# Kernel tuning notes

Measured on AMD Instinct MI355X. Metric: run time of the kernel, lower is better.

## Reference

```python
import jax, jax.numpy as jnp
import numpy as np

D = 256
B, S, N = 4, 512, 4


def setup_inputs() -> dict:
    key = jax.random.key(0)
    ks = jax.random.split(key, 24)
    d, dq = D, D // 4
    std = 0.02
    inp = {
        'x':   jax.random.normal(ks[0], (B, S, N, d), jnp.float32),
        'Wq':  jax.random.normal(ks[1], (d, d), jnp.float32) * std,
        'Wk':  jax.random.normal(ks[2], (d, d), jnp.float32) * std,
        'Wv':  jax.random.normal(ks[3], (d, d), jnp.float32) * std,
        'Wg1': jax.random.normal(ks[4], (d, d), jnp.float32) * std,
        'bg1': jnp.zeros((d,), jnp.float32),
        'Wg2': jax.random.normal(ks[5], (d, d), jnp.float32) * std,
        'bg2': jnp.zeros((d,), jnp.float32),
        'We1': jax.random.normal(ks[6], (d, dq), jnp.float32) * std,
        'be1': jnp.zeros((dq,), jnp.float32),
        'We2': jax.random.normal(ks[7], (dq, 1), jnp.float32) * std,
        'be2': jnp.zeros((1,), jnp.float32),
        'Wa1': jax.random.normal(ks[8], (d, dq), jnp.float32) * std,
        'ba1': jnp.zeros((dq,), jnp.float32),
        'Wa2': jax.random.normal(ks[9], (dq, 1), jnp.float32) * std,
        'ba2': jnp.zeros((1,), jnp.float32),
        'Wo':  jax.random.normal(ks[10], (d, d), jnp.float32) * std,
        'bo':  jnp.zeros((d,), jnp.float32),
        'gamma': jnp.ones((d,), jnp.float32),
        'beta':  jnp.zeros((d,), jnp.float32),
    }
    return inp


def reference(x, Wq, Wk, Wv, Wg1, bg1, Wg2, bg2, We1, be1, We2, be2,
              Wa1, ba1, Wa2, ba2, Wo, bo, gamma, beta):
    b, s, n, f = x.shape
    xf = x.reshape(b * n, s, f)  # matches torch .view on contiguous x
    residual = xf

    q = xf @ Wq                                    # [bn, s, d]
    k = xf @ Wk
    v = xf @ Wv
    v_hat = jax.nn.silu(v @ Wg1 + bg1) @ Wg2 + bg2  # value_generator
    eta = jax.nn.sigmoid(jax.nn.silu(xf @ We1 + be1) @ We2 + be2) * 0.1 + 0.01   # [bn, s, 1]
    alpha = jax.nn.sigmoid(jax.nn.silu(xf @ Wa1 + ba1) @ Wa2 + ba2) * 0.5 + 0.5  # [bn, s, 1]

    # F.normalize(k, dim=-1): eps = 1e-12
    kn = k / jnp.maximum(jnp.linalg.norm(k, axis=-1, keepdims=True), 1e-12)

    M0 = jnp.zeros((b * n, f, f), x.dtype)

    def step(M, inp):
        q_t, k_t, v_t, e_t, a_t = inp  # [bn,d],[bn,d],[bn,d],[bn,1],[bn,1]
        out_t = jnp.einsum('bij,bj->bi', M, q_t)
        Mk = jnp.einsum('bij,bj->bi', M, k_t)
        e = e_t[:, :, None]  # [bn,1,1]
        a = a_t[:, :, None]
        # delta rule: M <- a*M - e*(Mk k^T) + e*(v k^T)
        M_new = a * M + e * ((v_t - Mk)[:, :, None] * k_t[:, None, :])
        return M_new, out_t

    seq = (jnp.swapaxes(q, 0, 1), jnp.swapaxes(kn, 0, 1), jnp.swapaxes(v_hat, 0, 1),
           jnp.swapaxes(eta, 0, 1), jnp.swapaxes(alpha, 0, 1))
    M, outs = jax.lax.scan(step, M0, seq)
    out = jnp.swapaxes(outs, 0, 1)  # [bn, s, d]

    y = out @ Wo + bo + residual  # dropout is identity in eval/reference
    mu = jnp.mean(y, axis=-1, keepdims=True)
    var = jnp.var(y, axis=-1, keepdims=True)
    y = (y - mu) / jnp.sqrt(var + 1e-5) * gamma + beta
    return y.reshape(b, s, n, f), M
```

## Files before the change

### kernel.cpp

```cpp
#include <hip/hip_runtime.h>

#define F_ 256
#define S_ 512
#define NH_ 16
#define CCH 32
#define NCH (S_/CCH)
#define KSTR 264
#define KTSTR 36
#define TSTR 40

typedef __attribute__((ext_vector_type(8))) short short8_t;
typedef __attribute__((ext_vector_type(4))) float f32x4;

#define BARX() do { \
  asm volatile("s_waitcnt lgkmcnt(0)" ::: "memory"); \
  __builtin_amdgcn_s_barrier(); \
  __builtin_amdgcn_sched_barrier(0); \
} while (0)

__device__ __forceinline__ float sigmoid_f(float x) { return 1.0f / (1.0f + __expf(-x)); }

__device__ __forceinline__ ushort f2bf(float x) {
  uint u = __float_as_uint(x);
  u += 0x7FFFu + ((u >> 16) & 1u);
  return (ushort)(u >> 16);
}
__device__ __forceinline__ float bf2f(ushort u) {
  return __uint_as_float((uint)u << 16);
}

template<int CTRL>
__device__ __forceinline__ float dpp_add(float x) {
  int y = __builtin_amdgcn_update_dpp(0, __float_as_int(x), CTRL, 0xf, 0xf, true);
  return x + __int_as_float(y);
}
__device__ __forceinline__ float red8(float x) {
  x = dpp_add<0xB1>(x);
  x = dpp_add<0x4E>(x);
  x = dpp_add<0x141>(x);
  return x;
}

__global__ __launch_bounds__(256) void wconv_k(
    const float* __restrict__ Wq, const float* __restrict__ Wk,
    const float* __restrict__ Wv, const float* __restrict__ Wg1,
    const float* __restrict__ Wg2, const float* __restrict__ Wo,
    const float* __restrict__ We1, const float* __restrict__ Wa1,
    const float* __restrict__ be1, const float* __restrict__ ba1,
    ushort* __restrict__ Wt, float* __restrict__ beas)
{
  const int blk = blockIdx.x, tid = threadIdx.x;
  if (blk == 104) {
    if (tid < 64) beas[tid] = be1[tid];
    else if (tid < 128) beas[tid] = ba1[tid - 64];
    return;
  }
  __shared__ float tile[64][65];
  const float* src; int N, k0, n0; size_t dstbase;
  if (blk < 96) {
    const int w = blk >> 4, tl = blk & 15;
    const float* ws_[6] = {Wq, Wk, Wv, Wg1, Wg2, Wo};
    const size_t dstb[6] = {0, 65536, 131072, 229376, 294912, 360448};
    src = ws_[w]; N = 256;
    k0 = (tl >> 2) * 64; n0 = (tl & 3) * 64;
    dstbase = dstb[w];
  } else {
    const int w = (blk - 96) >> 2, tl = (blk - 96) & 3;
    src = w ? Wa1 : We1; N = 64;
    k0 = tl * 64; n0 = 0;
    dstbase = w ? 212992 : 196608;
  }
  #pragma unroll
  for (int p = 0; p < 4; ++p) {
    const int idx = (p << 8) + tid;
    const int r = idx >> 4, c4 = (idx & 15) << 2;
    if (c4 < N) {
      const float4 v = *(const float4*)&src[(size_t)(k0 + r) * N + n0 + c4];
      tile[r][c4 + 0] = v.x; tile[r][c4 + 1] = v.y;
      tile[r][c4 + 2] = v.z; tile[r][c4 + 3] = v.w;
    }
  }
  __syncthreads();
  #pragma unroll
  for (int p = 0; p < 4; ++p) {
    const int idx = (p << 8) + tid;
    const int nl = idx >> 4, kc = (idx & 15) << 2;
    if ((n0 + nl) < ((blk < 96) ? 256 : 64)) {
      ushort4 o;
      o.x = f2bf(tile[kc + 0][nl]); o.y = f2bf(tile[kc + 1][nl]);
      o.z = f2bf(tile[kc + 2][nl]); o.w = f2bf(tile[kc + 3][nl]);
      *(ushort4*)&Wt[dstbase + (size_t)(n0 + nl) * 256 + k0 + kc] = o;
    }
  }
}

__global__ __launch_bounds__(256) void qkve_k(
    const float* __restrict__ x, const ushort* __restrict__ Wt,
    const float* __restrict__ beas,
    ushort* __restrict__ qb, float* __restrict__ kf,
    ushort* __restrict__ vb, float* __restrict__ sesa)
{
  __shared__ ushort As[2][64 * 72];
  __shared__ ushort Ws[2][64 * 72];
  const int tid = threadIdx.x;
  const int wv = tid >> 6, l = tid & 63;
  const int ln = l & 15, hi = l >> 4, hi4 = hi << 2, hi8 = hi << 3;
  const int wr = wv >> 1, wc = wv & 1;
  const int row0 = blockIdx.y * 64, col0 = blockIdx.x * 64;
  const int r_ = tid >> 3, c8_ = (tid & 7) << 3;

  float4 pAf[4];
  short8_t pB[2];
  auto loadT = [&](int k0) {
    pAf[0] = *(const float4*)&x[(size_t)(row0 + r_) * 256 + k0 + c8_];
    pAf[1] = *(const float4*)&x[(size_t)(row0 + r_) * 256 + k0 + c8_ + 4];
    pAf[2] = *(const float4*)&x[(size_t)(row0 + 32 + r_) * 256 + k0 + c8_];
    pAf[3] = *(const float4*)&x[(size_t)(row0 + 32 + r_) * 256 + k0 + c8_ + 4];
    pB[0] = *(const short8_t*)&Wt[(size_t)(col0 + r_) * 256 + k0 + c8_];
    pB[1] = *(const short8_t*)&Wt[(size_t)(col0 + 32 + r_) * 256 + k0 + c8_];
  };
  auto commitT = [&](int b) {
    #pragma unroll
    for (int h = 0; h < 2; ++h) {
      short8_t s;
      s[0] = (short)f2bf(pAf[h*2].x); s[1] = (short)f2bf(pAf[h*2].y);
      s[2] = (short)f2bf(pAf[h*2].z); s[3] = (short)f2bf(pAf[h*2].w);
      s[4] = (short)f2bf(pAf[h*2+1].x); s[5] = (short)f2bf(pAf[h*2+1].y);
      s[6] = (short)f2bf(pAf[h*2+1].z); s[7] = (short)f2bf(pAf[h*2+1].w);
      *(short8_t*)&As[b][(h * 32 + r_) * 72 + c8_] = s;
    }
    *(short8_t*)&Ws[b][r_ * 72 + c8_] = pB[0];
    *(short8_t*)&Ws[b][(32 + r_) * 72 + c8_] = pB[1];
  };

  f32x4 acc[2][2];
  #pragma unroll
  for (int i = 0; i < 2; ++i)
    #pragma unroll
    for (int j = 0; j < 2; ++j)
      #pragma unroll
      for (int r = 0; r < 4; ++r) acc[i][j][r] = 0.f;

  loadT(0); commitT(0); __syncthreads();
  #pragma unroll
  for (int t = 0; t < 4; ++t) {
    const int b = t & 1;
    if (t < 3) loadT((t + 1) << 6);
    #pragma unroll
    for (int kk = 0; kk < 2; ++kk) {
      short8_t a0 = *(const short8_t*)&As[b][(wr * 32 + ln) * 72 + kk * 32 + hi8];
      short8_t a1 = *(const short8_t*)&As[b][(wr * 32 + 16 + ln) * 72 + kk * 32 + hi8];
      short8_t b0 = *(const short8_t*)&Ws[b][(wc * 32 + ln) * 72 + kk * 32 + hi8];
      short8_t b1 = *(const short8_t*)&Ws[b][(wc * 32 + 16 + ln) * 72 + kk * 32 + hi8];
      acc[0][0] = __builtin_amdgcn_mfma_f32_16x16x32_bf16(a0, b0, acc[0][0], 0, 0, 0);
      acc[0][1] = __builtin_amdgcn_mfma_f32_16x16x32_bf16(a0, b1, acc[0][1], 0, 0, 0);
      acc[1][0] = __builtin_amdgcn_mfma_f32_16x16x32_bf16(a1, b0, acc[1][0], 0, 0, 0);
      acc[1][1] = __builtin_amdgcn_mfma_f32_16x16x32_bf16(a1, b1, acc[1][1], 0, 0, 0);
    }
    if (t < 3) commitT(b ^ 1);
    __syncthreads();
  }

  #pragma unroll
  for (int mi = 0; mi < 2; ++mi)
    #pragma unroll
    for (int ni = 0; ni < 2; ++ni) {
      const int col = col0 + wc * 32 + ni * 16 + ln;
      #pragma unroll
      for (int r = 0; r < 4; ++r) {
        const int row = row0 + wr * 32 + mi * 16 + hi4 + r;
        float vx = acc[mi][ni][r];
        if (col0 < 256)      qb[(size_t)row * 256 + col] = f2bf(vx);
        else if (col0 < 512) kf[(size_t)row * 256 + (col - 256)] = vx;
        else if (col0 < 768) vb[(size_t)row * 256 + (col - 512)] = f2bf(vx);
        else {
          const int cc = col - 768;
          vx += beas[cc];
          vx *= sigmoid_f(vx);
          sesa[(size_t)row * 128 + cc] = vx;
        }
      }
    }
}

__global__ __launch_bounds__(256) void gemm_bf16_k(
    const ushort* __restrict__ A, const ushort* __restrict__ Wt,
    const float* __restrict__ bias, float* __restrict__ Cf,
    ushort* __restrict__ Cb, int act)
{
  __shared__ ushort As[2][64 * 72];
  __shared__ ushort Ws[2][64 * 72];
  const int tid = threadIdx.x;
  const int wv = tid >> 6, l = tid & 63;
  const int ln = l & 15, hi = l >> 4, hi4 = hi << 2, hi8 = hi << 3;
  const int wr = wv >> 1, wc = wv & 1;
  const int row0 = blockIdx.y * 64, col0 = blockIdx.x * 64;
  const int r_ = tid >> 3, c8_ = (tid & 7) << 3;

  short8_t pA[2], pB[2];
  auto loadT = [&](int k0) {
    pA[0] = *(const short8_t*)&A[(size_t)(row0 + r_) * 256 + k0 + c8_];
    pA[1] = *(const short8_t*)&A[(size_t)(row0 + 32 + r_) * 256 + k0 + c8_];
    pB[0] = *(const short8_t*)&Wt[(size_t)(col0 + r_) * 256 + k0 + c8_];
    pB[1] = *(const short8_t*)&Wt[(size_t)(col0 + 32 + r_) * 256 + k0 + c8_];
  };
  auto commitT = [&](int b) {
    *(short8_t*)&As[b][r_ * 72 + c8_] = pA[0];
    *(short8_t*)&As[b][(32 + r_) * 72 + c8_] = pA[1];
    *(short8_t*)&Ws[b][r_ * 72 + c8_] = pB[0];
    *(short8_t*)&Ws[b][(32 + r_) * 72 + c8_] = pB[1];
  };

  f32x4 acc[2][2];
  #pragma unroll
  for (int i = 0; i < 2; ++i)
    #pragma unroll
    for (int j = 0; j < 2; ++j)
      #pragma unroll
      for (int r = 0; r < 4; ++r) acc[i][j][r] = 0.f;

  loadT(0); commitT(0); __syncthreads();
  #pragma unroll
  for (int t = 0; t < 4; ++t) {
    const int b = t & 1;
    if (t < 3) loadT((t + 1) << 6);
    #pragma unroll
    for (int kk = 0; kk < 2; ++kk) {
      short8_t a0 = *(const short8_t*)&As[b][(wr * 32 + ln) * 72 + kk * 32 + hi8];
      short8_t a1 = *(const short8_t*)&As[b][(wr * 32 + 16 + ln) * 72 + kk * 32 + hi8];
      short8_t b0 = *(const short8_t*)&Ws[b][(wc * 32 + ln) * 72 + kk * 32 + hi8];
      short8_t b1 = *(const short8_t*)&Ws[b][(wc * 32 + 16 + ln) * 72 + kk * 32 + hi8];
      acc[0][0] = __builtin_amdgcn_mfma_f32_16x16x32_bf16(a0, b0, acc[0][0], 0, 0, 0);
      acc[0][1] = __builtin_amdgcn_mfma_f32_16x16x32_bf16(a0, b1, acc[0][1], 0, 0, 0);
      acc[1][0] = __builtin_amdgcn_mfma_f32_16x16x32_bf16(a1, b0, acc[1][0], 0, 0, 0);
      acc[1][1] = __builtin_amdgcn_mfma_f32_16x16x32_bf16(a1, b1, acc[1][1], 0, 0, 0);
    }
    if (t < 3) commitT(b ^ 1);
    __syncthreads();
  }

  #pragma unroll
  for (int mi = 0; mi < 2; ++mi)
    #pragma unroll
    for (int ni = 0; ni < 2; ++ni) {
      const int col = col0 + wc * 32 + ni * 16 + ln;
      const float bval = bias ? bias[col] : 0.f;
      #pragma unroll
      for (int r = 0; r < 4; ++r) {
        const int row = row0 + wr * 32 + mi * 16 + hi4 + r;
        float vx = acc[mi][ni][r] + bval;
        if (act == 1) vx = vx * sigmoid_f(vx);
        if (Cf) Cf[(size_t)row * 256 + col] = vx;
        if (Cb) Cb[(size_t)row * 256 + col] = f2bf(vx);
      }
    }
}

__global__ __launch_bounds__(256) void g1prep_k(
    const ushort* __restrict__ vb, const ushort* __restrict__ WtG1,
    const float* __restrict__ bg1, ushort* __restrict__ t1b,
    const ushort* __restrict__ kb, const ushort* __restrict__ qb,
    const float* __restrict__ eta, const float* __restrict__ alpha,
    ushort* __restrict__ Tg, ushort* __restrict__ Gqg, float* __restrict__ Sg,
    ushort* __restrict__ Ktg)
{
  __shared__ __align__(16) char smem[38592];
  const int blk = blockIdx.x;
  const int tid = threadIdx.x;
  const int l = tid & 63, wv = tid >> 6;
  const int ln = l & 15, hi = l >> 4, hi4 = hi << 2, hi8 = hi << 3;

  if (blk < 512) {
    ushort* As = (ushort*)smem;
    ushort* Ws = (ushort*)(smem + 18432);
    const int wr = wv >> 1, wc = wv & 1;
    const int row0 = (blk >> 2) * 64, col0 = (blk & 3) * 64;
    const int r_ = tid >> 3, c8_ = (tid & 7) << 3;

    short8_t pA[2], pB[2];
    auto loadT = [&](int k0) {
      pA[0] = *(const short8_t*)&vb[(size_t)(row0 + r_) * 256 + k0 + c8_];
      pA[1] = *(const short8_t*)&vb[(size_t)(row0 + 32 + r_) * 256 + k0 + c8_];
      pB[0] = *(const short8_t*)&WtG1[(size_t)(col0 + r_) * 256 + k0 + c8_];
      pB[1] = *(const short8_t*)&WtG1[(size_t)(col0 + 32 + r_) * 256 + k0 + c8_];
    };
    auto commitT = [&](int b) {
      *(short8_t*)&As[b * 4608 + r_ * 72 + c8_] = pA[0];
      *(short8_t*)&As[b * 4608 + (32 + r_) * 72 + c8_] = pA[1];
      *(short8_t*)&Ws[b * 4608 + r_ * 72 + c8_] = pB[0];
      *(short8_t*)&Ws[b * 4608 + (32 + r_) * 72 + c8_] = pB[1];
    };

    f32x4 acc[2][2];
    #pragma unroll
    for (int i = 0; i < 2; ++i)
      #pragma unroll
      for (int j = 0; j < 2; ++j)
        #pragma unroll
        for (int r = 0; r < 4; ++r) acc[i][j][r] = 0.f;

    loadT(0); commitT(0); __syncthreads();
    #pragma unroll
    for (int t = 0; t < 4; ++t) {
      const int b = t & 1;
      if (t < 3) loadT((t + 1) << 6);
      #pragma unroll
      for (int kk = 0; kk < 2; ++kk) {
        short8_t a0 = *(const short8_t*)&As[b * 4608 + (wr * 32 + ln) * 72 + kk * 32 + hi8];
        short8_t a1 = *(const short8_t*)&As[b * 4608 + (wr * 32 + 16 + ln) * 72 + kk * 32 + hi8];
        short8_t b0 = *(const short8_t*)&Ws[b * 4608 + (wc * 32 + ln) * 72 + kk * 32 + hi8];
        short8_t b1 = *(const short8_t*)&Ws[b * 4608 + (wc * 32 + 16 + ln) * 72 + kk * 32 + hi8];
        acc[0][0] = __builtin_amdgcn_mfma_f32_16x16x32_bf16(a0, b0, acc[0][0], 0, 0, 0);
        acc[0][1] = __builtin_amdgcn_mfma_f32_16x16x32_bf16(a0, b1, acc[0][1], 0, 0, 0);
        acc[1][0] = __builtin_amdgcn_mfma_f32_16x16x32_bf16(a1, b0, acc[1][0], 0, 0, 0);
        acc[1][1] = __builtin_amdgcn_mfma_f32_16x16x32_bf16(a1, b1, acc[1][1], 0, 0, 0);
      }
      if (t < 3) commitT(b ^ 1);
      __syncthreads();
    }

    #pragma unroll
    for (int mi = 0; mi < 2; ++mi)
      #pragma unroll
      for (int ni = 0; ni < 2; ++ni) {
        const int col = col0 + wc * 32 + ni * 16 + ln;
        const float bval = bg1[col];
        #pragma unroll
        for (int r = 0; r < 4; ++r) {
          const int row = row0 + wr * 32 + mi * 16 + hi4 + r;
          float vx = acc[mi][ni][r] + bval;
          vx = vx * sigmoid_f(vx);
          t1b[(size_t)row * 256 + col] = f2bf(vx);
        }
      }
    return;
  }

  const int pb = blk - 512;
  const int ch = pb & 15, h = pb >> 4;
  const int t0 = ch * CCH;
  ushort* K_lds = (ushort*)smem;
  ushort* Q_lds = (ushort*)(smem + 16896);
  float*  G_lds = (float*)(smem + 33792);
  float*  ea    = (float*)(smem + 37888);
  float*  eaA   = (float*)(smem + 37888 + 0);
  float*  scal  = (float*)(smem + 38144);

  const ushort* kg = kb + (size_t)(h * S_ + t0) * F_;
  const ushort* qg = qb + (size_t)(h * S_ + t0) * F_;
  #pragma unroll
  for (int w = 0; w < 4; ++w) {
    int o = w * 256 + tid; int t = o >> 5, c8 = (o & 31) << 3;
    *(short8_t*)&K_lds[t * KSTR + c8] = *(const short8_t*)&kg[(size_t)t * F_ + c8];
    *(short8_t*)&Q_lds[t * KSTR + c8] = *(const short8_t*)&qg[(size_t)t * F_ + c8];
  }
  if (tid < CCH)            ea[tid] = eta[(size_t)h * S_ + t0 + tid];
  else if (tid < 2 * CCH)   ea[tid] = alpha[(size_t)h * S_ + t0 + tid - CCH];
  __syncthreads();
  (void)eaA;

  {
    const int tt = tid & 31, cl = tid >> 5;
    for (int cp = 0; cp < 32; ++cp) {
      const int c = cp * 8 + cl;
      Ktg[((size_t)h * F_ + c) * S_ + t0 + tt] = K_lds[tt * KSTR + c];
    }
  }

  {
    const int tI = wv >> 1, tJ = wv & 1;
    f32x4 accG = {0.f, 0.f, 0.f, 0.f};
    f32x4 accQ = {0.f, 0.f, 0.f, 0.f};
    #pragma unroll
    for (int ko = 0; ko < 8; ++ko) {
      const int cb = ko * 32 + hi8;
      short8_t bfr = *(const short8_t*)&K_lds[(tJ * 16 + ln) * KSTR + cb];
      short8_t aK  = *(const short8_t*)&K_lds[(tI * 16 + ln) * KSTR + cb];
      short8_t aQ  = *(const short8_t*)&Q_lds[(tI * 16 + ln) * KSTR + cb];
      accG = __builtin_amdgcn_mfma_f32_16x16x32_bf16(aK, bfr, accG, 0, 0, 0);
      accQ = __builtin_amdgcn_mfma_f32_16x16x32_bf16(aQ, bfr, accQ, 0, 0, 0);
    }
    ushort* Gqo = Gqg + (size_t)(h * NCH + ch) * (CCH * CCH);
    #pragma unroll
    for (int r = 0; r < 4; ++r) {
      const int t = tI * 16 + hi4 + r, s = tJ * 16 + ln;
      G_lds[t * CCH + s] = accG[r];
      Gqo[t * CCH + s] = (s < t) ? f2bf(accQ[r]) : (ushort)0;
    }
  }
  if (tid == 0) {
    float gp = 1.f;
    for (int t = 0; t < CCH; ++t) {
      const float a = ea[CCH + t], e = ea[t];
      const float gm = gp * a;
      scal[t]           = e / a;
      scal[CCH + t]     = e / gm;
      scal[2 * CCH + t] = gp;
      gp = gm;
    }
    scal[3 * CCH] = gp;
  }
  __syncthreads();

  {
    const int j = tid >> 3, g = tid & 7;
    float x0 = 0.f, x1 = 0.f, x2 = 0.f, x3 = 0.f;
    ushort* To = Tg + (size_t)(h * NCH + ch) * (CCH * CCH);
    #pragma unroll
    for (int t = 0; t < CCH; ++t) {
      float p = 0.f;
      const f32x4 gr = *(const f32x4*)&G_lds[t * CCH + 4 * g];
      if (4 * g + 0 < t) p += gr[0] * x0;
      if (4 * g + 1 < t) p += gr[1] * x1;
      if (4 * g + 2 < t) p += gr[2] * x2;
      if (4 * g + 3 < t) p += gr[3] * x3;
      const float tot = red8(p);
      const float xt = ((t == j) ? 1.f : 0.f) - scal[t] * tot;
      if (g == (t >> 2)) {
        if ((t & 3) == 0) x0 = xt; else if ((t & 3) == 1) x1 = xt;
        else if ((t & 3) == 2) x2 = xt; else x3 = xt;
      }
      if (g == 0) To[t * CCH + j] = f2bf(xt);
    }
  }
  if (tid < 97) Sg[(size_t)(h * NCH + ch) * 128 + tid] = scal[tid];
}

__global__ __launch_bounds__(256) void gemmo_ln_k(
    const ushort* __restrict__ A, const ushort* __restrict__ Wt,
    const float* __restrict__ bo, const float* __restrict__ x,
    const float* __restrict__ gamma, const float* __restrict__ beta,
    float* __restrict__ y)
{
  __shared__ ushort As[2][32 * 72];
  __shared__ ushort Ws[2][256 * 72];
  __shared__ float rs_[2][32];
  __shared__ float rq_[2][32];
  const int tid = threadIdx.x;
  const int wv = tid >> 6, l = tid & 63;
  const int ln = l & 15, hi = l >> 4, hi4 = hi << 2, hi8 = hi << 3;
  const int g = wv >> 1, chf = wv & 1;
  const int row0 = blockIdx.x * 32;

  short8_t pA, pW[8];
  auto loadT = [&](int k0) {
    { const int r = tid >> 3, c8 = (tid & 7) << 3;
      pA = *(const short8_t*)&A[(size_t)(row0 + r) * 256 + k0 + c8]; }
    #pragma unroll
    for (int p = 0; p < 8; ++p) {
      const int idx = (p << 8) + tid;
      const int n = idx >> 3, c8 = (idx & 7) << 3;
      pW[p] = *(const short8_t*)&Wt[(size_t)n * 256 + k0 + c8];
    }
  };
  auto commitT = [&](int b) {
    { const int r = tid >> 3, c8 = (tid & 7) << 3;
      *(short8_t*)&As[b][r * 72 + c8] = pA; }
    #pragma unroll
    for (int p = 0; p < 8; ++p) {
      const int idx = (p << 8) + tid;
      const int n = idx >> 3, c8 = (idx & 7) << 3;
      *(short8_t*)&Ws[b][n * 72 + c8] = pW[p];
    }
  };

  f32x4 acc[8];
  #pragma unroll
  for (int nt = 0; nt < 8; ++nt)
    #pragma unroll
    for (int r = 0; r < 4; ++r) acc[nt][r] = 0.f;

  loadT(0); commitT(0); __syncthreads();
  #pragma unroll
  for (int t = 0; t < 4; ++t) {
    const int b = t & 1;
    if (t < 3) loadT((t + 1) << 6);
    #pragma unroll
    for (int kk = 0; kk < 2; ++kk) {
      short8_t a = *(const short8_t*)&As[b][(g * 16 + ln) * 72 + kk * 32 + hi8];
      #pragma unroll
      for (int nt = 0; nt < 8; ++nt) {
        short8_t bb = *(const short8_t*)&Ws[b][(chf * 128 + nt * 16 + ln) * 72 + kk * 32 + hi8];
        acc[nt] = __builtin_amdgcn_mfma_f32_16x16x32_bf16(a, bb, acc[nt], 0, 0, 0);
      }
    }
    if (t < 3) commitT(b ^ 1);
    __syncthreads();
  }

  float val[8][4];
  float sm[4] = {0.f, 0.f, 0.f, 0.f}, sq[4] = {0.f, 0.f, 0.f, 0.f};
  #pragma unroll
  for (int nt = 0; nt < 8; ++nt) {
    const int col = chf * 128 + nt * 16 + ln;
    const float bv = bo[col];
    #pragma unroll
    for (int r = 0; r < 4; ++r) {
      const int row = row0 + g * 16 + hi4 + r;
      const float v = acc[nt][r] + bv + x[(size_t)row * 256 + col];
      val[nt][r] = v;
      sm[r] += v;
      sq[r] += v * v;
    }
  }
  #pragma unroll
  for (int m = 1; m < 16; m <<= 1) {
    #pragma unroll
    for (int r = 0; r < 4; ++r) {
      sm[r] += __shfl_xor(sm[r], m, 64);
      sq[r] += __shfl_xor(sq[r], m, 64);
    }
  }
  if (ln == 0) {
    #pragma unroll
    for (int r = 0; r < 4; ++r) {
      rs_[chf][g * 16 + hi4 + r] = sm[r];
      rq_[chf][g * 16 + hi4 + r] = sq[r];
    }
  }
  __syncthreads();
  #pragma unroll
  for (int r = 0; r < 4; ++r) {
    const int lr = g * 16 + hi4 + r;
    const float tot = rs_[0][lr] + rs_[1][lr];
    const float tq  = rq_[0][lr] + rq_[1][lr];
    const float mu  = tot * (1.0f / 256.0f);
    const float var = tq * (1.0f / 256.0f) - mu * mu;
    const float rstd = rsqrtf(var + 1e-5f);
    #pragma unroll
    for (int nt = 0; nt < 8; ++nt) {
      const int col = chf * 128 + nt * 16 + ln;
      y[(size_t)(row0 + lr) * 256 + col] =
          (val[nt][r] - mu) * rstd * gamma[col] + beta[col];
    }
  }
}

__global__ __launch_bounds__(256) void knea_k(
    const float* __restrict__ kf, ushort* __restrict__ kb,
    const float* __restrict__ sesa,
    const float* __restrict__ We2, const float* __restrict__ be2,
    const float* __restrict__ Wa2, const float* __restrict__ ba2,
    float* __restrict__ eta, float* __restrict__ alpha)
{
  const int lane = threadIdx.x & 63;
  const size_t row = ((size_t)blockIdx.x << 2) + (threadIdx.x >> 6);
  {
    const size_t off = row * F_ + ((size_t)lane << 2);
    float4 v = *(const float4*)&kf[off];
    float ss = v.x * v.x + v.y * v.y + v.z * v.z + v.w * v.w;
    #pragma unroll
    for (int m = 1; m < 64; m <<= 1) ss += __shfl_xor(ss, m, 64);
    const float sc = 1.0f / fmaxf(sqrtf(ss), 1e-12f);
    ushort4 o;
    o.x = f2bf(v.x * sc); o.y = f2bf(v.y * sc);
    o.z = f2bf(v.z * sc); o.w = f2bf(v.w * sc);
    *(ushort4*)&kb[off] = o;
  }
  {
    float pe = sesa[row * 128 + lane] * We2[lane];
    float pa = sesa[row * 128 + 64 + lane] * Wa2[lane];
    #pragma unroll
    for (int m = 1; m < 64; m <<= 1) {
      pe += __shfl_xor(pe, m, 64);
      pa += __shfl_xor(pa, m, 64);
    }
    if (lane == 0) {
      eta[row]   = sigmoid_f(pe + be2[0]) * 0.1f + 0.01f;
      alpha[row] = sigmoid_f(pa + ba2[0]) * 0.5f + 0.5f;
    }
  }
}

__global__ __launch_bounds__(256, 1) void scan_chunk_k(
    const ushort* __restrict__ kb, const ushort* __restrict__ qb,
    const ushort* __restrict__ vhb, const ushort* __restrict__ Ktg,
    const ushort* __restrict__ Tg, const ushort* __restrict__ Gqg,
    const float* __restrict__ Sg,
    ushort* __restrict__ outb, float* __restrict__ Mout)
{
  __shared__ ushort K_lds[2][CCH * KSTR];
  __shared__ ushort Q_lds[2][CCH * KSTR];
  __shared__ ushort Kt_lds[2][F_ * KTSTR];
  __shared__ ushort M_lds[16 * KSTR];
  __shared__ ushort T_lds[2][CCH * TSTR];
  __shared__ ushort Gq_lds[2][CCH * TSTR];
  __shared__ ushort Wt_lds[16 * TSTR];
  __shared__ ushort R2_lds[2][16 * TSTR];
  __shared__ float  QM_lds[CCH * 20];
  __shared__ ushort V_lds[2][CCH * 16];
  __shared__ float  scal[2][104];

  const int tid = threadIdx.x;
  const int flat = blockIdx.x;
  const int h = (flat & 7) + (((flat >> 3) >> 4) << 3);
  const int slice = (flat >> 3) & 15;
  const int r0 = slice * 16;
  const int wv = tid >> 6, l = tid & 63;
  const int ln = l & 15, hi = l >> 4, hi4 = hi << 2, hi8 = hi << 3;

  for (int u = tid; u < 16 * KSTR / 8; u += 256) {
    short8_t z = {0, 0, 0, 0, 0, 0, 0, 0};
    *(short8_t*)&M_lds[u * 8] = z;
  }
  f32x4 Mf[4];
  #pragma unroll
  for (int q = 0; q < 4; ++q)
    #pragma unroll
    for (int r = 0; r < 4; ++r) Mf[q][r] = 0.f;

  const ushort* kgh = kb + (size_t)h * S_ * F_;
  const ushort* qgh = qb + (size_t)h * S_ * F_;
  const ushort* kth = Ktg + (size_t)h * F_ * S_;

  short8_t pK[4], pQ[4], pKt[4], pTG;
  ushort pV[2]; float pS = 0.f;

  auto loadchunk = [&](int ch) {
    const int t0 = ch * CCH;
    #pragma unroll
    for (int r = 0; r < 4; ++r) {
      const int idx = (r << 8) + tid;
      const int t = idx >> 5, c8 = (idx & 31) << 3;
      pK[r] = *(const short8_t*)&kgh[(size_t)(t0 + t) * F_ + c8];
      pQ[r] = *(const short8_t*)&qgh[(size_t)(t0 + t) * F_ + c8];
    }
    #pragma unroll
    for (int r = 0; r < 4; ++r) {
      const int idx = (r << 8) + tid;
      const int c = idx >> 2, t8 = (idx & 3) << 3;
      pKt[r] = *(const short8_t*)&kth[(size_t)c * S_ + t0 + t8];
    }
    #pragma unroll
    for (int u = 0; u < 2; ++u) {
      const int e = (u << 8) + tid, t = e >> 4, i = e & 15;
      pV[u] = vhb[(size_t)(h * S_ + t0 + t) * F_ + r0 + i];
    }
    {
      const ushort* Ti = Tg  + (size_t)(h * NCH + ch) * (CCH * CCH);
      const ushort* Gi = Gqg + (size_t)(h * NCH + ch) * (CCH * CCH);
      if (tid < 128) {
        const int t = tid >> 2, c8 = (tid & 3) << 3;
        pTG = *(const short8_t*)&Ti[t * CCH + c8];
      } else {
        const int t = (tid - 128) >> 2, c8 = ((tid - 128) & 3) << 3;
        pTG = *(const short8_t*)&Gi[t * CCH + c8];
      }
    }
    if (tid < 97) pS = Sg[(size_t)(h * NCH + ch) * 128 + tid];
  };

  auto commit = [&](int buf) {
    #pragma unroll
    for (int r = 0; r < 4; ++r) {
      const int idx = (r << 8) + tid;
      const int t = idx >> 5, c8 = (idx & 31) << 3;
      *(short8_t*)&K_lds[buf][t * KSTR + c8] = pK[r];
      *(short8_t*)&Q_lds[buf][t * KSTR + c8] = pQ[r];
    }
    #pragma unroll
    for (int r = 0; r < 4; ++r) {
      const int idx = (r << 8) + tid;
      const int c = idx >> 2, t8 = (idx & 3) << 3;
      *(short8_t*)&Kt_lds[buf][c * KTSTR + t8] = pKt[r];
    }
    #pragma unroll
    for (int u = 0; u < 2; ++u) V_lds[buf][(u << 8) + tid] = pV[u];
    if (tid < 128) {
      const int t = tid >> 2, c8 = (tid & 3) << 3;
      *(short8_t*)&T_lds[buf][t * TSTR + c8] = pTG;
    } else {
      const int t = (tid - 128) >> 2, c8 = ((tid - 128) & 3) << 3;
      *(short8_t*)&Gq_lds[buf][t * TSTR + c8] = pTG;
    }
    if (tid < 97) scal[buf][tid] = pS;
  };

  loadchunk(0);
  commit(0);
  BARX();

  for (int ch = 0; ch < NCH; ++ch) {
    const int buf = ch & 1;
    const int t0 = ch * CCH;
    if (ch + 1 < NCH) loadchunk(ch + 1);

    if (wv < 2) {
      #pragma unroll
      for (int tt = 0; tt < 2; ++tt) {
        f32x4 a0 = {0.f, 0.f, 0.f, 0.f}, a1 = {0.f, 0.f, 0.f, 0.f};
        #pragma unroll
        for (int ko = 0; ko < 4; ++ko) {
          {
            short8_t a = *(const short8_t*)&K_lds[buf][(tt * 16 + ln) * KSTR + (2 * ko) * 32 + hi8];
            short8_t b = *(const short8_t*)&M_lds[ln * KSTR + (2 * ko) * 32 + hi8];
            a0 = __builtin_amdgcn_mfma_f32_16x16x32_bf16(a, b, a0, 0, 0, 0);
          }
          {
            short8_t a = *(const short8_t*)&K_lds[buf][(tt * 16 + ln) * KSTR + (2 * ko + 1) * 32 + hi8];
            short8_t b = *(const short8_t*)&M_lds[ln * KSTR + (2 * ko + 1) * 32 + hi8];
            a1 = __builtin_amdgcn_mfma_f32_16x16x32_bf16(a, b, a1, 0, 0, 0);
          }
        }
        #pragma unroll
        for (int r = 0; r < 4; ++r) {
          const int t = tt * 16 + hi4 + r;
          const float s = a0[r] + a1[r];
          const float rhs = scal[buf][CCH + t] * bf2f(V_lds[buf][t * 16 + ln])
                          - scal[buf][t] * s;
          R2_lds[wv][ln * TSTR + t] = f2bf(rhs);
        }
      }
      asm volatile("s_waitcnt lgkmcnt(0)" ::: "memory");
      __builtin_amdgcn_sched_barrier(0);
      {
        const int I = wv;
        short8_t a = *(const short8_t*)&T_lds[buf][(I * 16 + ln) * TSTR + hi8];
        short8_t b = *(const short8_t*)&R2_lds[wv][ln * TSTR + hi8];
        f32x4 z = {0.f, 0.f, 0.f, 0.f};
        f32x4 d = __builtin_amdgcn_mfma_f32_16x16x32_bf16(a, b, z, 0, 0, 0);
        #pragma unroll
        for (int r = 0; r < 4; ++r)
          Wt_lds[ln * TSTR + I * 16 + hi4 + r] = f2bf(d[r]);
      }
    } else {
      const int I = wv - 2;
      f32x4 a0 = {0.f, 0.f, 0.f, 0.f}, a1 = {0.f, 0.f, 0.f, 0.f};
      #pragma unroll
      for (int ko = 0; ko < 4; ++ko) {
        {
          short8_t a = *(const short8_t*)&Q_lds[buf][(I * 16 + ln) * KSTR + (2 * ko) * 32 + hi8];
          short8_t b = *(const short8_t*)&M_lds[ln * KSTR + (2 * ko) * 32 + hi8];
          a0 = __builtin_amdgcn_mfma_f32_16x16x32_bf16(a, b, a0, 0, 0, 0);
        }
        {
          short8_t a = *(const short8_t*)&Q_lds[buf][(I * 16 + ln) * KSTR + (2 * ko + 1) * 32 + hi8];
          short8_t b = *(const short8_t*)&M_lds[ln * KSTR + (2 * ko + 1) * 32 + hi8];
          a1 = __builtin_amdgcn_mfma_f32_16x16x32_bf16(a, b, a1, 0, 0, 0);
        }
      }
      #pragma unroll
      for (int r = 0; r < 4; ++r)
        QM_lds[(I * 16 + hi4 + r) * 20 + ln] = a0[r] + a1[r];
    }
    BARX();

    {
      const float gC = scal[buf][3 * CCH];
      short8_t aw = *(const short8_t*)&Wt_lds[ln * TSTR + hi8];
      #pragma unroll
      for (int qq = 0; qq < 4; ++qq) {
        const int jt = wv * 4 + qq;
        short8_t bk = *(const short8_t*)&Kt_lds[buf][(jt * 16 + ln) * KTSTR + hi8];
        f32x4 d = __builtin_amdgcn_mfma_f32_16x16x32_bf16(aw, bk, Mf[qq], 0, 0, 0);
        #pragma unroll
        for (int r = 0; r < 4; ++r) {
          const float nv = gC * d[r];
          Mf[qq][r] = nv;
          M_lds[(hi4 + r) * KSTR + jt * 16 + ln] = f2bf(nv);
        }
      }
    }
    if (wv < 2) {
      const int I = wv;
      short8_t a = *(const short8_t*)&Gq_lds[buf][(I * 16 + ln) * TSTR + hi8];
      short8_t b = *(const short8_t*)&Wt_lds[ln * TSTR + hi8];
      f32x4 z = {0.f, 0.f, 0.f, 0.f};
      f32x4 d = __builtin_amdgcn_mfma_f32_16x16x32_bf16(a, b, z, 0, 0, 0);
      #pragma unroll
      for (int r = 0; r < 4; ++r) {
        const int t = I * 16 + hi4 + r;
        outb[(size_t)(h * S_ + t0 + t) * F_ + r0 + ln] =
            f2bf(scal[buf][2 * CCH + t] * (QM_lds[t * 20 + ln] + d[r]));
      }
    }
    if (ch + 1 < NCH) commit(buf ^ 1);
    BARX();
  }

  #pragma unroll
  for (int qq = 0; qq < 4; ++qq) {
    const int jt = wv * 4 + qq;
    #pragma unroll
    for (int r = 0; r < 4; ++r)
      Mout[((size_t)h * F_ + r0 + hi4 + r) * F_ + jt * 16 + ln] = Mf[qq][r];
  }
}

extern "C" void kernel_launch(void* const* d_in, const int* in_sizes, int n_in,
                              void* d_out, int out_size, void* d_ws, size_t ws_size,
                              hipStream_t stream)
{
  const float* x    = (const float*)d_in[0];
  const float* Wq   = (const float*)d_in[1];
  const float* Wk   = (const float*)d_in[2];
  const float* Wv   = (const float*)d_in[3];
  const float* Wg1  = (const float*)d_in[4];
  const float* bg1  = (const float*)d_in[5];
  const float* Wg2  = (const float*)d_in[6];
  const float* bg2  = (const float*)d_in[7];
  const float* We1  = (const float*)d_in[8];
  const float* be1  = (const float*)d_in[9];
  const float* We2  = (const float*)d_in[10];
  const float* be2  = (const float*)d_in[11];
  const float* Wa1  = (const float*)d_in[12];
  const float* ba1  = (const float*)d_in[13];
  const float* Wa2  = (const float*)d_in[14];
  const float* ba2  = (const float*)d_in[15];
  const float* Wo   = (const float*)d_in[16];
  const float* bo   = (const float*)d_in[17];
  const float* gamma= (const float*)d_in[18];
  const float* beta = (const float*)d_in[19];

  const int Mrows = NH_ * S_;
  const size_t MM = 1048576;
  const size_t NTF = 2 * MM;

  float* ws = (float*)d_ws;
  ushort* outb = (ushort*)(ws + 0 * MM);
  ushort* qb   = (ushort*)(ws + 1 * MM);
  ushort* kb   = (ushort*)(ws + 2 * MM);
  float*  kf   = ws + 3 * MM;
  ushort* t1b  = (ushort*)(ws + 3 * MM);
  ushort* vhb  = (ushort*)(ws + 4 * MM);
  ushort* vb   = (ushort*)(ws + 5 * MM);
  float*  sesa = ws + 6 * MM;
  float*  eta  = ws + 7 * MM;
  float*  alpha= eta + Mrows;
  ushort* Tg   = (ushort*)(ws + 7 * MM + 16384);
  ushort* Gqg  = Tg + 262144;
  float*  Sg   = ws + 7 * MM + 16384 + 131072 + 131072;
  ushort* Ktg  = (ushort*)(Sg + 32768);
  ushort* Wt   = Ktg + 2097152;
  float*  beas = (float*)(Wt + 425984);

  dim3 blk(256);

  wconv_k<<<105, blk, 0, stream>>>(Wq, Wk, Wv, Wg1, Wg2, Wo, We1, Wa1,
                                   be1, ba1, Wt, beas);

  qkve_k<<<dim3(14, 128), blk, 0, stream>>>(x, Wt, beas, qb, kf, vb, sesa);

  knea_k<<<Mrows / 4, blk, 0, stream>>>(kf, kb, sesa, We2, be2, Wa2, ba2, eta, alpha);

  g1prep_k<<<768, blk, 0, stream>>>(vb, Wt + 229376, bg1, t1b,
                                    kb, qb, eta, alpha, Tg, Gqg, Sg, Ktg);

  gemm_bf16_k<<<dim3(4, 128), blk, 0, stream>>>(t1b, Wt + 294912, bg2, nullptr, vhb, 0);

  float* yout = (float*)d_out;
  float* Mfin = yout + NTF;
  scan_chunk_k<<<256, blk, 0, stream>>>(kb, qb, vhb, Ktg, Tg, Gqg, Sg, outb, Mfin);

  gemmo_ln_k<<<256, blk, 0, stream>>>(outb, Wt + 360448, bo, x, gamma, beta, yout);
}
```

Measured before the change: 96.81 us.

## Load scan operands straight into MFMA register fragments, drop LDS staging

The chunked scan kernel no longer stages K, Q, K^T, T, Gq, V and the scalars through double-buffered LDS. Each wave now loads its own MFMA operand fragments straight from global memory into registers, ping-ponging between two fragment sets across an unrolled pair of chunks. This removes the LDS commit writes and the re-reads, and cuts shared memory use. In exchange it adds an extra barrier per chunk (three instead of two), much higher register pressure, and less coalesced, fragment-shaped global loads (for example strided K^T rows).

```diff
diff --git a/kernel.cpp b/kernel.cpp
--- a/kernel.cpp
+++ b/kernel.cpp
@@ -6,7 +6,6 @@
 #define CCH 32
 #define NCH (S_/CCH)
 #define KSTR 264
-#define KTSTR 36
 #define TSTR 40
 
 typedef __attribute__((ext_vector_type(8))) short short8_t;
@@ -343,7 +342,6 @@
   ushort* Q_lds = (ushort*)(smem + 16896);
   float*  G_lds = (float*)(smem + 33792);
   float*  ea    = (float*)(smem + 37888);
-  float*  eaA   = (float*)(smem + 37888 + 0);
   float*  scal  = (float*)(smem + 38144);
 
   const ushort* kg = kb + (size_t)(h * S_ + t0) * F_;
@@ -357,7 +355,6 @@
   if (tid < CCH)            ea[tid] = eta[(size_t)h * S_ + t0 + tid];
   else if (tid < 2 * CCH)   ea[tid] = alpha[(size_t)h * S_ + t0 + tid - CCH];
   __syncthreads();
-  (void)eaA;
 
   {
     const int tt = tid & 31, cl = tid >> 5;
@@ -579,17 +576,10 @@
     const float* __restrict__ Sg,
     ushort* __restrict__ outb, float* __restrict__ Mout)
 {
-  __shared__ ushort K_lds[2][CCH * KSTR];
-  __shared__ ushort Q_lds[2][CCH * KSTR];
-  __shared__ ushort Kt_lds[2][F_ * KTSTR];
   __shared__ ushort M_lds[16 * KSTR];
-  __shared__ ushort T_lds[2][CCH * TSTR];
-  __shared__ ushort Gq_lds[2][CCH * TSTR];
   __shared__ ushort Wt_lds[16 * TSTR];
-  __shared__ ushort R2_lds[2][16 * TSTR];
+  __shared__ ushort R_lds[16 * TSTR];
   __shared__ float  QM_lds[CCH * 20];
-  __shared__ ushort V_lds[2][CCH * 16];
-  __shared__ float  scal[2][104];
 
   const int tid = threadIdx.x;
   const int flat = blockIdx.x;
@@ -612,170 +602,127 @@
   const ushort* kgh = kb + (size_t)h * S_ * F_;
   const ushort* qgh = qb + (size_t)h * S_ * F_;
   const ushort* kth = Ktg + (size_t)h * F_ * S_;
-
-  short8_t pK[4], pQ[4], pKt[4], pTG;
-  ushort pV[2]; float pS = 0.f;
-
-  auto loadchunk = [&](int ch) {
+  const ushort* vgh = vhb + (size_t)h * S_ * F_;
+
+  struct Frags {
+    short8_t P[8];
+    short8_t Kt[4];
+    short8_t T, Gq;
+    ushort   V[4];
+    float    b[4], c[4], gp[4];
+    float    gC;
+  };
+  Frags fA, fB;
+
+  auto loadchunk = [&](int ch, Frags& f) {
     const int t0 = ch * CCH;
-    #pragma unroll
-    for (int r = 0; r < 4; ++r) {
-      const int idx = (r << 8) + tid;
-      const int t = idx >> 5, c8 = (idx & 31) << 3;
-      pK[r] = *(const short8_t*)&kgh[(size_t)(t0 + t) * F_ + c8];
-      pQ[r] = *(const short8_t*)&qgh[(size_t)(t0 + t) * F_ + c8];
-    }
-    #pragma unroll
-    for (int r = 0; r < 4; ++r) {
-      const int idx = (r << 8) + tid;
-      const int c = idx >> 2, t8 = (idx & 3) << 3;
-      pKt[r] = *(const short8_t*)&kth[(size_t)c * S_ + t0 + t8];
-    }
-    #pragma unroll
-    for (int u = 0; u < 2; ++u) {
-      const int e = (u << 8) + tid, t = e >> 4, i = e & 15;
-      pV[u] = vhb[(size_t)(h * S_ + t0 + t) * F_ + r0 + i];
-    }
+    if (wv < 2) {
+      #pragma unroll
+      for (int ko = 0; ko < 8; ++ko)
+        f.P[ko] = *(const short8_t*)&kgh[(size_t)(t0 + wv * 16 + ln) * F_ + ko * 32 + hi8];
+      const size_t tb = (size_t)(h * NCH + ch) * (CCH * CCH);
+      f.T  = *(const short8_t*)&Tg [tb + (size_t)(wv * 16 + ln) * CCH + hi8];
+      f.Gq = *(const short8_t*)&Gqg[tb + (size_t)(wv * 16 + ln) * CCH + hi8];
+      const size_t sb = (size_t)(h * NCH + ch) * 128;
+      #pragma unroll
+      for (int r = 0; r < 4; ++r) {
+        const int t = wv * 16 + hi4 + r;
+        f.V[r]  = vgh[(size_t)(t0 + t) * F_ + r0 + ln];
+        f.b[r]  = Sg[sb + t];
+        f.c[r]  = Sg[sb + 32 + t];
+        f.gp[r] = Sg[sb + 64 + t];
+      }
+    } else {
+      #pragma unroll
+      for (int ko = 0; ko < 8; ++ko)
+        f.P[ko] = *(const short8_t*)&qgh[(size_t)(t0 + (wv - 2) * 16 + ln) * F_ + ko * 32 + hi8];
+    }
+    #pragma unroll
+    for (int qq = 0; qq < 4; ++qq)
+      f.Kt[qq] = *(const short8_t*)&kth[(size_t)((wv * 4 + qq) * 16 + ln) * S_ + t0 + hi8];
+    f.gC = Sg[(size_t)(h * NCH + ch) * 128 + 96];
+  };
+
+  auto CHUNK = [&](int ch, const Frags& f) {
+    const int t0 = ch * CCH;
+    if (wv < 2) {
+      f32x4 a0 = {0.f, 0.f, 0.f, 0.f}, a1 = {0.f, 0.f, 0.f, 0.f};
+      #pragma unroll
+      for (int ko = 0; ko < 4; ++ko) {
+        short8_t b0 = *(const short8_t*)&M_lds[ln * KSTR + (2 * ko) * 32 + hi8];
+        a0 = __builtin_amdgcn_mfma_f32_16x16x32_bf16(f.P[2 * ko], b0, a0, 0, 0, 0);
+        short8_t b1 = *(const short8_t*)&M_lds[ln * KSTR + (2 * ko + 1) * 32 + hi8];
+        a1 = __builtin_amdgcn_mfma_f32_16x16x32_bf16(f.P[2 * ko + 1], b1, a1, 0, 0, 0);
+      }
+      ushort4 rw;
+      float rv[4];
+      #pragma unroll
+      for (int r = 0; r < 4; ++r) {
+        const float s = a0[r] + a1[r];
+        rv[r] = f.c[r] * bf2f(f.V[r]) - f.b[r] * s;
+      }
+      rw.x = f2bf(rv[0]); rw.y = f2bf(rv[1]); rw.z = f2bf(rv[2]); rw.w = f2bf(rv[3]);
+      *(ushort4*)&R_lds[ln * TSTR + wv * 16 + hi4] = rw;
+    } else {
+      f32x4 a0 = {0.f, 0.f, 0.f, 0.f}, a1 = {0.f, 0.f, 0.f, 0.f};
+      #pragma unroll
+      for (int ko = 0; ko < 4; ++ko) {
+        short8_t b0 = *(const short8_t*)&M_lds[ln * KSTR + (2 * ko) * 32 + hi8];
+        a0 = __builtin_amdgcn_mfma_f32_16x16x32_bf16(f.P[2 * ko], b0, a0, 0, 0, 0);
+        short8_t b1 = *(const short8_t*)&M_lds[ln * KSTR + (2 * ko + 1) * 32 + hi8];
+        a1 = __builtin_amdgcn_mfma_f32_16x16x32_bf16(f.P[2 * ko + 1], b1, a1, 0, 0, 0);
+      }
+      #pragma unroll
+      for (int r = 0; r < 4; ++r)
+        QM_lds[((wv - 2) * 16 + hi4 + r) * 20 + ln] = a0[r] + a1[r];
+    }
+    BARX();
+
+    if (wv < 2) {
+      short8_t bfr = *(const short8_t*)&R_lds[ln * TSTR + hi8];
+      f32x4 z = {0.f, 0.f, 0.f, 0.f};
+      f32x4 d = __builtin_amdgcn_mfma_f32_16x16x32_bf16(f.T, bfr, z, 0, 0, 0);
+      ushort4 wo;
+      wo.x = f2bf(d[0]); wo.y = f2bf(d[1]); wo.z = f2bf(d[2]); wo.w = f2bf(d[3]);
+      *(ushort4*)&Wt_lds[ln * TSTR + wv * 16 + hi4] = wo;
+    }
+    BARX();
+
     {
-      const ushort* Ti = Tg  + (size_t)(h * NCH + ch) * (CCH * CCH);
-      const ushort* Gi = Gqg + (size_t)(h * NCH + ch) * (CCH * CCH);
-      if (tid < 128) {
-        const int t = tid >> 2, c8 = (tid & 3) << 3;
-        pTG = *(const short8_t*)&Ti[t * CCH + c8];
-      } else {
-        const int t = (tid - 128) >> 2, c8 = ((tid - 128) & 3) << 3;
-        pTG = *(const short8_t*)&Gi[t * CCH + c8];
-      }
-    }
-    if (tid < 97) pS = Sg[(size_t)(h * NCH + ch) * 128 + tid];
-  };
-
-  auto commit = [&](int buf) {
-    #pragma unroll
-    for (int r = 0; r < 4; ++r) {
-      const int idx = (r << 8) + tid;
-      const int t = idx >> 5, c8 = (idx & 31) << 3;
-      *(short8_t*)&K_lds[buf][t * KSTR + c8] = pK[r];
-      *(short8_t*)&Q_lds[buf][t * KSTR + c8] = pQ[r];
-    }
-    #pragma unroll
-    for (int r = 0; r < 4; ++r) {
-      const int idx = (r << 8) + tid;
-      const int c = idx >> 2, t8 = (idx & 3) << 3;
-      *(short8_t*)&Kt_lds[buf][c * KTSTR + t8] = pKt[r];
-    }
-    #pragma unroll
-    for (int u = 0; u < 2; ++u) V_lds[buf][(u << 8) + tid] = pV[u];
-    if (tid < 128) {
-      const int t = tid >> 2, c8 = (tid & 3) << 3;
-      *(short8_t*)&T_lds[buf][t * TSTR + c8] = pTG;
-    } else {
-      const int t = (tid - 128) >> 2, c8 = ((tid - 128) & 3) << 3;
-      *(short8_t*)&Gq_lds[buf][t * TSTR + c8] = pTG;
-    }
-    if (tid < 97) scal[buf][tid] = pS;
-  };
-
-  loadchunk(0);
-  commit(0);
-  BARX();
-
-  for (int ch = 0; ch < NCH; ++ch) {
-    const int buf = ch & 1;
-    const int t0 = ch * CCH;
-    if (ch + 1 < NCH) loadchunk(ch + 1);
-
-    if (wv < 2) {
-      #pragma unroll
-      for (int tt = 0; tt < 2; ++tt) {
-        f32x4 a0 = {0.f, 0.f, 0.f, 0.f}, a1 = {0.f, 0.f, 0.f, 0.f};
-        #pragma unroll
-        for (int ko = 0; ko < 4; ++ko) {
-          {
-            short8_t a = *(const short8_t*)&K_lds[buf][(tt * 16 + ln) * KSTR + (2 * ko) * 32 + hi8];
-            short8_t b = *(const short8_t*)&M_lds[ln * KSTR + (2 * ko) * 32 + hi8];
-            a0 = __builtin_amdgcn_mfma_f32_16x16x32_bf16(a, b, a0, 0, 0, 0);
-          }
-          {
-            short8_t a = *(const short8_t*)&K_lds[buf][(tt * 16 + ln) * KSTR + (2 * ko + 1) * 32 + hi8];
-            short8_t b = *(const short8_t*)&M_lds[ln * KSTR + (2 * ko + 1) * 32 + hi8];
-            a1 = __builtin_amdgcn_mfma_f32_16x16x32_bf16(a, b, a1, 0, 0, 0);
-          }
-        }
+      short8_t aw = *(const short8_t*)&Wt_lds[ln * TSTR + hi8];
+      #pragma unroll
+      for (int qq = 0; qq < 4; ++qq) {
+        const int jt = wv * 4 + qq;
+        f32x4 d = __builtin_amdgcn_mfma_f32_16x16x32_bf16(aw, f.Kt[qq], Mf[qq], 0, 0, 0);
         #pragma unroll
         for (int r = 0; r < 4; ++r) {
-          const int t = tt * 16 + hi4 + r;
-          const float s = a0[r] + a1[r];
-          const float rhs = scal[buf][CCH + t] * bf2f(V_lds[buf][t * 16 + ln])
-                          - scal[buf][t] * s;
-          R2_lds[wv][ln * TSTR + t] = f2bf(rhs);
-        }
-      }
-      asm volatile("s_waitcnt lgkmcnt(0)" ::: "memory");
-      __builtin_amdgcn_sched_barrier(0);
-      {
-        const int I = wv;
-        short8_t a = *(const short8_t*)&T_lds[buf][(I * 16 + ln) * TSTR + hi8];
-        short8_t b = *(const short8_t*)&R2_lds[wv][ln * TSTR + hi8];
-        f32x4 z = {0.f, 0.f, 0.f, 0.f};
-        f32x4 d = __builtin_amdgcn_mfma_f32_16x16x32_bf16(a, b, z, 0, 0, 0);
-        #pragma unroll
-        for (int r = 0; r < 4; ++r)
-          Wt_lds[ln * TSTR + I * 16 + hi4 + r] = f2bf(d[r]);
-      }
-    } else {
-      const int I = wv - 2;
-      f32x4 a0 = {0.f, 0.f, 0.f, 0.f}, a1 = {0.f, 0.f, 0.f, 0.f};
-      #pragma unroll
-      for (int ko = 0; ko < 4; ++ko) {
-        {
-          short8_t a = *(const short8_t*)&Q_lds[buf][(I * 16 + ln) * KSTR + (2 * ko) * 32 + hi8];
-          short8_t b = *(const short8_t*)&M_lds[ln * KSTR + (2 * ko) * 32 + hi8];
-          a0 = __builtin_amdgcn_mfma_f32_16x16x32_bf16(a, b, a0, 0, 0, 0);
-        }
-        {
-          short8_t a = *(const short8_t*)&Q_lds[buf][(I * 16 + ln) * KSTR + (2 * ko + 1) * 32 + hi8];
-          short8_t b = *(const short8_t*)&M_lds[ln * KSTR + (2 * ko + 1) * 32 + hi8];
-          a1 = __builtin_amdgcn_mfma_f32_16x16x32_bf16(a, b, a1, 0, 0, 0);
-        }
-      }
-      #pragma unroll
-      for (int r = 0; r < 4; ++r)
-        QM_lds[(I * 16 + hi4 + r) * 20 + ln] = a0[r] + a1[r];
-    }
-    BARX();
-
-    {
-      const float gC = scal[buf][3 * CCH];
-      short8_t aw = *(const short8_t*)&Wt_lds[ln * TSTR + hi8];
-      #pragma unroll
-      for (int qq = 0; qq < 4; ++qq) {
-        const int jt = wv * 4 + qq;
-        short8_t bk = *(const short8_t*)&Kt_lds[buf][(jt * 16 + ln) * KTSTR + hi8];
-        f32x4 d = __builtin_amdgcn_mfma_f32_16x16x32_bf16(aw, bk, Mf[qq], 0, 0, 0);
-        #pragma unroll
-        for (int r = 0; r < 4; ++r) {
-          const float nv = gC * d[r];
+          const float nv = f.gC * d[r];
           Mf[qq][r] = nv;
           M_lds[(hi4 + r) * KSTR + jt * 16 + ln] = f2bf(nv);
         }
       }
-    }
-    if (wv < 2) {
-      const int I = wv;
-      short8_t a = *(const short8_t*)&Gq_lds[buf][(I * 16 + ln) * TSTR + hi8];
-      short8_t b = *(const short8_t*)&Wt_lds[ln * TSTR + hi8];
-      f32x4 z = {0.f, 0.f, 0.f, 0.f};
-      f32x4 d = __builtin_amdgcn_mfma_f32_16x16x32_bf16(a, b, z, 0, 0, 0);
-      #pragma unroll
-      for (int r = 0; r < 4; ++r) {
-        const int t = I * 16 + hi4 + r;
-        outb[(size_t)(h * S_ + t0 + t) * F_ + r0 + ln] =
-            f2bf(scal[buf][2 * CCH + t] * (QM_lds[t * 20 + ln] + d[r]));
-      }
-    }
-    if (ch + 1 < NCH) commit(buf ^ 1);
+      if (wv < 2) {
+        f32x4 z = {0.f, 0.f, 0.f, 0.f};
+        f32x4 d = __builtin_amdgcn_mfma_f32_16x16x32_bf16(f.Gq, aw, z, 0, 0, 0);
+        #pragma unroll
+        for (int r = 0; r < 4; ++r) {
+          const int t = wv * 16 + hi4 + r;
+          outb[(size_t)(h * S_ + t0 + t) * F_ + r0 + ln] =
+              f2bf(f.gp[r] * (QM_lds[t * 20 + ln] + d[r]));
+        }
+      }
+    }
     BARX();
+  };
+
+  loadchunk(0, fA);
+  BARX();
+
+  for (int ch = 0; ch < NCH; ch += 2) {
+    loadchunk(ch + 1, fB);
+    CHUNK(ch, fA);
+    if (ch + 2 < NCH) loadchunk(ch + 2, fA);
+    CHUNK(ch + 1, fB);
   }
 
   #pragma unroll
```

New measurement: 100.4 us. 3.7% more time.

## Split K·M work across waves with an extra barrier and raise wave priority

Applied to the files above, without the earlier changes.

Waves 0-1 each compute their own 16-row K·M tile and write one shared R buffer, instead of each computing both tiles redundantly. An extra __syncthreads is added before the T·R MFMA produces Wt. The Gq·Wt output stage now runs before the M update, and s_setprio brackets the MFMA-heavy sections. The custom BARX barrier is replaced with plain __syncthreads. This halves the redundant MFMA work in waves 0-1 but adds a barrier per chunk on the serial scan path.

```diff
diff --git a/kernel.cpp b/kernel.cpp
--- a/kernel.cpp
+++ b/kernel.cpp
@@ -11,12 +11,6 @@
 
 typedef __attribute__((ext_vector_type(8))) short short8_t;
 typedef __attribute__((ext_vector_type(4))) float f32x4;
-
-#define BARX() do { \
-  asm volatile("s_waitcnt lgkmcnt(0)" ::: "memory"); \
-  __builtin_amdgcn_s_barrier(); \
-  __builtin_amdgcn_sched_barrier(0); \
-} while (0)
 
 __device__ __forceinline__ float sigmoid_f(float x) { return 1.0f / (1.0f + __expf(-x)); }
 
@@ -343,7 +337,6 @@
   ushort* Q_lds = (ushort*)(smem + 16896);
   float*  G_lds = (float*)(smem + 33792);
   float*  ea    = (float*)(smem + 37888);
-  float*  eaA   = (float*)(smem + 37888 + 0);
   float*  scal  = (float*)(smem + 38144);
 
   const ushort* kg = kb + (size_t)(h * S_ + t0) * F_;
@@ -357,7 +350,6 @@
   if (tid < CCH)            ea[tid] = eta[(size_t)h * S_ + t0 + tid];
   else if (tid < 2 * CCH)   ea[tid] = alpha[(size_t)h * S_ + t0 + tid - CCH];
   __syncthreads();
-  (void)eaA;
 
   {
     const int tt = tid & 31, cl = tid >> 5;
@@ -586,7 +578,7 @@
   __shared__ ushort T_lds[2][CCH * TSTR];
   __shared__ ushort Gq_lds[2][CCH * TSTR];
   __shared__ ushort Wt_lds[16 * TSTR];
-  __shared__ ushort R2_lds[2][16 * TSTR];
+  __shared__ ushort R_lds[16 * TSTR];
   __shared__ float  QM_lds[CCH * 20];
   __shared__ ushort V_lds[2][CCH * 16];
   __shared__ float  scal[2][104];
@@ -678,50 +670,37 @@
 
   loadchunk(0);
   commit(0);
-  BARX();
+  __syncthreads();
 
   for (int ch = 0; ch < NCH; ++ch) {
     const int buf = ch & 1;
     const int t0 = ch * CCH;
     if (ch + 1 < NCH) loadchunk(ch + 1);
 
+    __builtin_amdgcn_s_setprio(1);
     if (wv < 2) {
-      #pragma unroll
-      for (int tt = 0; tt < 2; ++tt) {
-        f32x4 a0 = {0.f, 0.f, 0.f, 0.f}, a1 = {0.f, 0.f, 0.f, 0.f};
-        #pragma unroll
-        for (int ko = 0; ko < 4; ++ko) {
-          {
-            short8_t a = *(const short8_t*)&K_lds[buf][(tt * 16 + ln) * KSTR + (2 * ko) * 32 + hi8];
-            short8_t b = *(const short8_t*)&M_lds[ln * KSTR + (2 * ko) * 32 + hi8];
-            a0 = __builtin_amdgcn_mfma_f32_16x16x32_bf16(a, b, a0, 0, 0, 0);
-          }
-          {
-            short8_t a = *(const short8_t*)&K_lds[buf][(tt * 16 + ln) * KSTR + (2 * ko + 1) * 32 + hi8];
-            short8_t b = *(const short8_t*)&M_lds[ln * KSTR + (2 * ko + 1) * 32 + hi8];
-            a1 = __builtin_amdgcn_mfma_f32_16x16x32_bf16(a, b, a1, 0, 0, 0);
-          }
+      const int I = wv;
+      f32x4 a0 = {0.f, 0.f, 0.f, 0.f}, a1 = {0.f, 0.f, 0.f, 0.f};
+      #pragma unroll
+      for (int ko = 0; ko < 4; ++ko) {
+        {
+          short8_t a = *(const short8_t*)&K_lds[buf][(I * 16 + ln) * KSTR + (2 * ko) * 32 + hi8];
+          short8_t b = *(const short8_t*)&M_lds[ln * KSTR + (2 * ko) * 32 + hi8];
+          a0 = __builtin_amdgcn_mfma_f32_16x16x32_bf16(a, b, a0, 0, 0, 0);
         }
-        #pragma unroll
-        for (int r = 0; r < 4; ++r) {
-          const int t = tt * 16 + hi4 + r;
-          const float s = a0[r] + a1[r];
-          const float rhs = scal[buf][CCH + t] * bf2f(V_lds[buf][t * 16 + ln])
-                          - scal[buf][t] * s;
-          R2_lds[wv][ln * TSTR + t] = f2bf(rhs);
+        {
+          short8_t a = *(const short8_t*)&K_lds[buf][(I * 16 + ln) * KSTR + (2 * ko + 1) * 32 + hi8];
+          short8_t b = *(const short8_t*)&M_lds[ln * KSTR + (2 * ko + 1) * 32 + hi8];
+          a1 = __builtin_amdgcn_mfma_f32_16x16x32_bf16(a, b, a1, 0, 0, 0);
         }
       }
-      asm volatile("s_waitcnt lgkmcnt(0)" ::: "memory");
-      __builtin_amdgcn_sched_barrier(0);
-      {
-        const int I = wv;
-        short8_t a = *(const short8_t*)&T_lds[buf][(I * 16 + ln) * TSTR + hi8];
-        short8_t b = *(const short8_t*)&R2_lds[wv][ln * TSTR + hi8];
-        f32x4 z = {0.f, 0.f, 0.f, 0.f};
-        f32x4 d = __builtin_amdgcn_mfma_f32_16x16x32_bf16(a, b, z, 0, 0, 0);
-        #pragma unroll
-        for (int r = 0; r < 4; ++r)
-          Wt_lds[ln * TSTR + I * 16 + hi4 + r] = f2bf(d[r]);
+      #pragma unroll
+      for (int r = 0; r < 4; ++r) {
+        const int t = I * 16 + hi4 + r;
+        const float s = a0[r] + a1[r];
+        const float rhs = scal[buf][CCH + t] * bf2f(V_lds[buf][t * 16 + ln])
+                        - scal[buf][t] * s;
+        R_lds[ln * TSTR + t] = f2bf(rhs);
       }
     } else {
       const int I = wv - 2;
@@ -743,8 +722,35 @@
       for (int r = 0; r < 4; ++r)
         QM_lds[(I * 16 + hi4 + r) * 20 + ln] = a0[r] + a1[r];
     }
-    BARX();
-
+    __builtin_amdgcn_s_setprio(0);
+    __syncthreads();
+
+    if (wv < 2) {
+      const int I = wv;
+      short8_t a = *(const short8_t*)&T_lds[buf][(I * 16 + ln) * TSTR + hi8];
+      short8_t b = *(const short8_t*)&R_lds[ln * TSTR + hi8];
+      f32x4 z = {0.f, 0.f, 0.f, 0.f};
+      f32x4 d = __builtin_amdgcn_mfma_f32_16x16x32_bf16(a, b, z, 0, 0, 0);
+      #pragma unroll
+      for (int r = 0; r < 4; ++r)
+        Wt_lds[ln * TSTR + I * 16 + hi4 + r] = f2bf(d[r]);
+    }
+    __syncthreads();
+
+    __builtin_amdgcn_s_setprio(1);
+    if (wv < 2) {
+      const int I = wv;
+      short8_t a = *(const short8_t*)&Gq_lds[buf][(I * 16 + ln) * TSTR + hi8];
+      short8_t b = *(const short8_t*)&Wt_lds[ln * TSTR + hi8];
+      f32x4 z = {0.f, 0.f, 0.f, 0.f};
+      f32x4 d = __builtin_amdgcn_mfma_f32_16x16x32_bf16(a, b, z, 0, 0, 0);
+      #pragma unroll
+      for (int r = 0; r < 4; ++r) {
+        const int t = I * 16 + hi4 + r;
+        outb[(size_t)(h * S_ + t0 + t) * F_ + r0 + ln] =
+            f2bf(scal[buf][2 * CCH + t] * (QM_lds[t * 20 + ln] + d[r]));
+      }
+    }
     {
       const float gC = scal[buf][3 * CCH];
       short8_t aw = *(const short8_t*)&Wt_lds[ln * TSTR + hi8];
@@ -761,21 +767,9 @@
         }
       }
     }
-    if (wv < 2) {
-      const int I = wv;
-      short8_t a = *(const short8_t*)&Gq_lds[buf][(I * 16 + ln) * TSTR + hi8];
-      short8_t b = *(const short8_t*)&Wt_lds[ln * TSTR + hi8];
-      f32x4 z = {0.f, 0.f, 0.f, 0.f};
-      f32x4 d = __builtin_amdgcn_mfma_f32_16x16x32_bf16(a, b, z, 0, 0, 0);
-      #pragma unroll
-      for (int r = 0; r < 4; ++r) {
-        const int t = I * 16 + hi4 + r;
-        outb[(size_t)(h * S_ + t0 + t) * F_ + r0 + ln] =
-            f2bf(scal[buf][2 * CCH + t] * (QM_lds[t * 20 + ln] + d[r]));
-      }
-    }
+    __builtin_amdgcn_s_setprio(0);
     if (ch + 1 < NCH) commit(buf ^ 1);
-    BARX();
+    __syncthreads();
   }
 
   #pragma unroll
```

Result: no change. 95.14 us (-1.7%).
